# Performance work log

Hardware: AMD Instinct MI355X
Metric: run time of the kernel (lower is better)

Reference implementation:

```python
import jax, jax.numpy as jnp
import numpy as np

A1, A2 = 16, 16            # block tile sizes (arr_size1, arr_size2)
G = 1000                   # graph_size (max node index + 1)
EG = 16000                 # number of graph edges (avg degree 16)
SIZE1 = G * A1             # input feature length  (16000)
SIZE2 = G * A2             # output feature length (16000)
NNZ = EG * A1 * A2         # expanded COO entries  (4,096,000)
B = 32                     # batch


def _expand_indices(t0, t1, a1, a2):
    """Vectorized adjust_indices: edge (t0,t1) -> tile of (row,col) pairs.
    row = t0*a2 + j, col = t1*a1 + i  for all i in [a1), j in [a2)."""
    e = t0.shape[0]
    j = np.arange(a2)
    i = np.arange(a1)
    rows = np.broadcast_to(t0[:, None, None] * a2 + j[None, None, :], (e, a1, a2)).reshape(-1)
    cols = np.broadcast_to(t1[:, None, None] * a1 + i[None, :, None], (e, a1, a2)).reshape(-1)
    return rows.astype(np.int32), cols.astype(np.int32)


def setup_inputs() -> dict:
    key = jax.random.key(0)
    ks = jax.random.split(key, 6)
    rng = np.random.default_rng(0)
    t0 = rng.integers(0, G, EG)
    t1 = rng.integers(0, G, EG)
    rows_np, cols_np = _expand_indices(t0, t1, A1, A2)
    # original init: uniform(-1/len(indices), 1/len(indices)) with len([2,nnz])==2 -> U(-0.5, 0.5)
    return {
        "x": jax.random.normal(ks[0], (B, SIZE1, 1), dtype=jnp.float32),
        "weight_mean": jax.random.uniform(ks[1], (NNZ,), jnp.float32, -0.5, 0.5),
        "weight_log_var": jnp.zeros((NNZ,), jnp.float32),
        "b_mean": jax.random.uniform(ks[2], (SIZE2,), jnp.float32, -0.5, 0.5),
        "b_log_var": jnp.zeros((SIZE2,), jnp.float32),
        "eps_w": jax.random.normal(ks[3], (NNZ,), dtype=jnp.float32),
        "eps_b": jax.random.normal(ks[4], (SIZE2,), dtype=jnp.float32),
        "rows": jnp.asarray(rows_np),
        "cols": jnp.asarray(cols_np),
    }


def reference(x, weight_mean, weight_log_var, b_mean, b_log_var, eps_w, eps_b, rows, cols):
    # reparameterization sample of sparse weight values
    values = eps_w * jnp.exp(weight_log_var) + weight_mean          # [NNZ]
    # COO spmm: out[b, r, k] += values[e] * x[b, c, k] for each (r, c) = (rows[e], cols[e])
    contrib = values[None, :, None] * x[:, cols, :]                 # [B, NNZ, 1]
    out = jnp.zeros((x.shape[0], SIZE2, x.shape[2]), x.dtype).at[:, rows, :].add(contrib)
    # reparameterized bias, broadcast over batch
    b = eps_b * jnp.exp(b_log_var) + b_mean                         # [SIZE2]
    out = out + b[None, :, None]
    # kl is explicitly zeroed in the source right before return
    return (out, jnp.asarray(0.0, dtype=x.dtype))
```

## Files before the change

### kernel.cpp

```cpp
#include <hip/hip_runtime.h>

#define EG   16000
#define NG   1000
#define BB   32
#define SIZE 16000


__global__ void count_kernel(const int* __restrict__ rows, int* __restrict__ cnt) {
    int e = blockIdx.x * blockDim.x + threadIdx.x;
    if (e < EG) {
        int t0 = rows[e << 8] >> 4;
        atomicAdd(&cnt[t0], 1);
    }
}

__global__ void scan_kernel(const int* __restrict__ cnt,
                            int* __restrict__ bin_start,
                            int* __restrict__ cursor) {
    __shared__ int s[1024];
    int t = threadIdx.x;
    int c = (t < NG) ? cnt[t] : 0;
    s[t] = c;
    __syncthreads();
    for (int off = 1; off < 1024; off <<= 1) {
        int v = (t >= off) ? s[t - off] : 0;
        __syncthreads();
        s[t] += v;
        __syncthreads();
    }
    int incl = s[t];
    if (t < NG) { bin_start[t] = incl - c; cursor[t] = incl - c; }
    if (t == 1023) bin_start[NG] = incl;
}

__global__ void scatter_kernel(const int* __restrict__ rows,
                               int* __restrict__ cursor,
                               int* __restrict__ edge_of) {
    int e = blockIdx.x * blockDim.x + threadIdx.x;
    if (e < EG) {
        int t0 = rows[e << 8] >> 4;
        int pos = atomicAdd(&cursor[t0], 1);
        edge_of[pos] = e;
    }
}


__global__ __launch_bounds__(256) void spmm_kernel(
    const float* __restrict__ wm, const float* __restrict__ wlv,
    const float* __restrict__ ew, const float* __restrict__ x,
    const float* __restrict__ bm, const float* __restrict__ blv,
    const float* __restrict__ eb, const int* __restrict__ cols,
    const int* __restrict__ edge_of, const int* __restrict__ bin_start,
    float* __restrict__ out)
{
    __shared__ float vt[256];
    __shared__ float xs[512];

    int g   = blockIdx.x;
    int tid = threadIdx.x;
    int j   = tid & 15;
    int b0  = tid >> 4;

    float acc0 = 0.f, acc1 = 0.f;
    int start = bin_start[g], end = bin_start[g + 1];

    for (int p = start; p < end; ++p) {
        int e    = edge_of[p];
        int base = e << 8;
        int t1   = cols[base] >> 4;
        vt[tid] = ew[base + tid] * __expf(wlv[base + tid]) + wm[base + tid];
        int xb = t1 << 4;
        xs[tid]       = x[ b0        * SIZE + xb + j];
        xs[tid + 256] = x[(b0 + 16)  * SIZE + xb + j];
        __syncthreads();
        #pragma unroll
        for (int i = 0; i < 16; ++i) {
            float vv = vt[(i << 4) + j];
            acc0 += vv * xs[((b0)      << 4) + i];
            acc1 += vv * xs[((b0 + 16) << 4) + i];
        }
        __syncthreads();
    }

    int r = (g << 4) + j;
    float bias = eb[r] * __expf(blv[r]) + bm[r];
    out[ b0       * SIZE + r] = acc0 + bias;
    out[(b0 + 16) * SIZE + r] = acc1 + bias;
    if (g == 0 && tid == 0) out[BB * SIZE] = 0.0f;
}

extern "C" void kernel_launch(void* const* d_in, const int* in_sizes, int n_in,
                              void* d_out, int out_size, void* d_ws, size_t ws_size,
                              hipStream_t stream) {
    const float* x   = (const float*)d_in[0];
    const float* wm  = (const float*)d_in[1];
    const float* wlv = (const float*)d_in[2];
    const float* bm  = (const float*)d_in[3];
    const float* blv = (const float*)d_in[4];
    const float* ew  = (const float*)d_in[5];
    const float* eb  = (const float*)d_in[6];
    const int* rows  = (const int*)d_in[7];
    const int* cols  = (const int*)d_in[8];
    float* out = (float*)d_out;

    char* ws = (char*)d_ws;
    int* cnt       = (int*)(ws);
    int* bin_start = (int*)(ws + 4096);
    int* cursor    = (int*)(ws + 8192);
    int* edge_of   = (int*)(ws + 12288);

    hipMemsetAsync(cnt, 0, 4096, stream);
    count_kernel<<<(EG + 255) / 256, 256, 0, stream>>>(rows, cnt);
    scan_kernel<<<1, 1024, 0, stream>>>(cnt, bin_start, cursor);
    scatter_kernel<<<(EG + 255) / 256, 256, 0, stream>>>(rows, cursor, edge_of);
    spmm_kernel<<<NG, 256, 0, stream>>>(wm, wlv, ew, x, bm, blv, eb, cols,
                                        edge_of, bin_start, out);
}
```

Baseline: 156.0 us.

## Precompute sampled weights in a separate pass and drop shared-memory staging in SpMM

Adds a vectorized prep kernel that computes the reparameterized weight values into a workspace buffer. The scatter step now packs each edge's column tile with its edge id, so the SpMM no longer gathers from cols. The SpMM is rewritten to 128 threads, with each thread loading x rows as float4 directly into registers and accumulating four batch outputs, removing the per-edge __syncthreads and shared-memory staging. The cost is an extra full write and reread of the 16 MB value array and more redundant x loads per thread.

```diff
diff --git a/kernel.cpp b/kernel.cpp
--- a/kernel.cpp
+++ b/kernel.cpp
@@ -4,7 +4,23 @@
 #define NG   1000
 #define BB   32
 #define SIZE 16000
+#define NNZ  (EG * 256)
 
+__global__ __launch_bounds__(256) void prep_kernel(
+    const float* __restrict__ wm, const float* __restrict__ wlv,
+    const float* __restrict__ ew, float* __restrict__ v)
+{
+    int k = blockIdx.x * 256 + threadIdx.x;
+    const float4 m = ((const float4*)wm)[k];
+    const float4 l = ((const float4*)wlv)[k];
+    const float4 e = ((const float4*)ew)[k];
+    float4 r;
+    r.x = fmaf(e.x, __expf(l.x), m.x);
+    r.y = fmaf(e.y, __expf(l.y), m.y);
+    r.z = fmaf(e.z, __expf(l.z), m.z);
+    r.w = fmaf(e.w, __expf(l.w), m.w);
+    ((float4*)v)[k] = r;
+}
 
 __global__ void count_kernel(const int* __restrict__ rows, int* __restrict__ cnt) {
     int e = blockIdx.x * blockDim.x + threadIdx.x;
@@ -34,58 +50,76 @@
 }
 
 __global__ void scatter_kernel(const int* __restrict__ rows,
+                               const int* __restrict__ cols,
                                int* __restrict__ cursor,
                                int* __restrict__ edge_of) {
     int e = blockIdx.x * blockDim.x + threadIdx.x;
     if (e < EG) {
         int t0 = rows[e << 8] >> 4;
+        int t1 = cols[e << 8] >> 4;
         int pos = atomicAdd(&cursor[t0], 1);
-        edge_of[pos] = e;
+        edge_of[pos] = e | (t1 << 16);
     }
 }
 
-
-__global__ __launch_bounds__(256) void spmm_kernel(
-    const float* __restrict__ wm, const float* __restrict__ wlv,
-    const float* __restrict__ ew, const float* __restrict__ x,
+__global__ __launch_bounds__(128) void spmm_kernel(
+    const float* __restrict__ v, const float* __restrict__ x,
     const float* __restrict__ bm, const float* __restrict__ blv,
-    const float* __restrict__ eb, const int* __restrict__ cols,
-    const int* __restrict__ edge_of, const int* __restrict__ bin_start,
-    float* __restrict__ out)
+    const float* __restrict__ eb, const int* __restrict__ edge_of,
+    const int* __restrict__ bin_start, float* __restrict__ out)
 {
-    __shared__ float vt[256];
-    __shared__ float xs[512];
-
+    __shared__ int hdr[256];
     int g   = blockIdx.x;
     int tid = threadIdx.x;
     int j   = tid & 15;
     int b0  = tid >> 4;
 
-    float acc0 = 0.f, acc1 = 0.f;
-    int start = bin_start[g], end = bin_start[g + 1];
+    int start = bin_start[g];
+    int n     = bin_start[g + 1] - start;
+    for (int t = tid; t < n && t < 256; t += 128) hdr[t] = edge_of[start + t];
+    __syncthreads();
 
-    for (int p = start; p < end; ++p) {
-        int e    = edge_of[p];
-        int base = e << 8;
-        int t1   = cols[base] >> 4;
-        vt[tid] = ew[base + tid] * __expf(wlv[base + tid]) + wm[base + tid];
-        int xb = t1 << 4;
-        xs[tid]       = x[ b0        * SIZE + xb + j];
-        xs[tid + 256] = x[(b0 + 16)  * SIZE + xb + j];
-        __syncthreads();
+    float a0 = 0.f, a1 = 0.f, a2 = 0.f, a3 = 0.f;
+
+    for (int p = 0; p < n; ++p) {
+        int h  = (p < 256) ? hdr[p] : edge_of[start + p];
+        int e  = h & 0xFFFF;
+        int t1 = h >> 16;
+        const float* wc = v + (e << 8) + j;
+        const float* xp = x + (t1 << 4);
+
+        float4 X0[4], X1[4], X2[4], X3[4];
+        #pragma unroll
+        for (int q = 0; q < 4; ++q) {
+            X0[q] = ((const float4*)(xp + (b0     ) * SIZE))[q];
+            X1[q] = ((const float4*)(xp + (b0 +  8) * SIZE))[q];
+            X2[q] = ((const float4*)(xp + (b0 + 16) * SIZE))[q];
+            X3[q] = ((const float4*)(xp + (b0 + 24) * SIZE))[q];
+        }
+        float W[16];
+        #pragma unroll
+        for (int i = 0; i < 16; ++i) W[i] = wc[i << 4];
+
+        const float* f0 = (const float*)X0;
+        const float* f1 = (const float*)X1;
+        const float* f2 = (const float*)X2;
+        const float* f3 = (const float*)X3;
         #pragma unroll
         for (int i = 0; i < 16; ++i) {
-            float vv = vt[(i << 4) + j];
-            acc0 += vv * xs[((b0)      << 4) + i];
-            acc1 += vv * xs[((b0 + 16) << 4) + i];
+            float wv = W[i];
+            a0 = fmaf(wv, f0[i], a0);
+            a1 = fmaf(wv, f1[i], a1);
+            a2 = fmaf(wv, f2[i], a2);
+            a3 = fmaf(wv, f3[i], a3);
         }
-        __syncthreads();
     }
 
     int r = (g << 4) + j;
-    float bias = eb[r] * __expf(blv[r]) + bm[r];
-    out[ b0       * SIZE + r] = acc0 + bias;
-    out[(b0 + 16) * SIZE + r] = acc1 + bias;
+    float bias = fmaf(eb[r], __expf(blv[r]), bm[r]);
+    out[(b0     ) * SIZE + r] = a0 + bias;
+    out[(b0 +  8) * SIZE + r] = a1 + bias;
+    out[(b0 + 16) * SIZE + r] = a2 + bias;
+    out[(b0 + 24) * SIZE + r] = a3 + bias;
     if (g == 0 && tid == 0) out[BB * SIZE] = 0.0f;
 }
 
@@ -104,15 +138,16 @@
     float* out = (float*)d_out;
 
     char* ws = (char*)d_ws;
-    int* cnt       = (int*)(ws);
-    int* bin_start = (int*)(ws + 4096);
-    int* cursor    = (int*)(ws + 8192);
-    int* edge_of   = (int*)(ws + 12288);
+    int*   cnt       = (int*)(ws);
+    int*   bin_start = (int*)(ws + 4096);
+    int*   cursor    = (int*)(ws + 8192);
+    int*   edge_of   = (int*)(ws + 12288);
+    float* v         = (float*)(ws + 131072);
 
     hipMemsetAsync(cnt, 0, 4096, stream);
+    prep_kernel<<<NNZ / 4 / 256, 256, 0, stream>>>(wm, wlv, ew, v);
     count_kernel<<<(EG + 255) / 256, 256, 0, stream>>>(rows, cnt);
     scan_kernel<<<1, 1024, 0, stream>>>(cnt, bin_start, cursor);
-    scatter_kernel<<<(EG + 255) / 256, 256, 0, stream>>>(rows, cursor, edge_of);
-    spmm_kernel<<<NG, 256, 0, stream>>>(wm, wlv, ew, x, bm, blv, eb, cols,
-                                        edge_of, bin_start, out);
+    scatter_kernel<<<(EG + 255) / 256, 256, 0, stream>>>(rows, cols, cursor, edge_of);
+    spmm_kernel<<<NG, 128, 0, stream>>>(v, x, bm, blv, eb, edge_of, bin_start, out);
 }
```

Result: slower. 161.8 us (+3.7%).
